# Performance work log

Measured on AMD Instinct MI355X. Metric: run time of the kernel, lower is better.

The kernel has to match this reference:

```python
import jax, jax.numpy as jnp
import numpy as np

B, T, D_IN, D, OUT, L, NDAYS = 32, 2048, 512, 256, 41, 3, 45
INNER = 2 * D  # expand=2

def silu(x):
    return x * jax.nn.sigmoid(x)

def layernorm(x, s, b, eps=1e-5):
    m = x.mean(-1, keepdims=True)
    v = ((x - m) ** 2).mean(-1, keepdims=True)
    return (x - m) / jnp.sqrt(v + eps) * s + b

def dwconv(x, k, b):
    # x: [B,T,C], k: [C,4] depthwise kernel, b: [C]
    # torch Conv1d(padding=2)[..., :T] == pad (left=2, right=1), valid window 4
    y = jax.lax.conv_general_dilated(
        x.transpose(0, 2, 1), k[:, None, :], window_strides=(1,),
        padding=[(2, 1)], feature_group_count=k.shape[0],
        dimension_numbers=('NCH', 'OIH', 'NCH'))
    return y.transpose(0, 2, 1) + b

def soft_window(x, Win, convK, convB, dtW, dtB, Wout):
    # x: [B,T,D]
    xz = x @ Win                      # [B,T,2*INNER]
    xi, z = jnp.split(xz, 2, axis=-1)
    xc = silu(dwconv(xi, convK, convB))
    dt = jax.nn.softplus(xc @ dtW + dtB)
    w = jnp.exp(-jnp.cumsum(dt, axis=1) * 0.1)
    return (xc * w * silu(z)) @ Wout  # [B,T,D]

def setup_inputs() -> dict:
    key = jax.random.key(0)
    ks = iter(jax.random.split(key, 40))
    n = lambda shp, s=0.02: jax.random.normal(next(ks), shp, dtype=jnp.float32) * s
    inp = {}
    inp['x'] = jax.random.normal(next(ks), (B, T, D_IN), dtype=jnp.float32)
    inp['day_ids'] = jax.random.randint(next(ks), (B,), 0, NDAYS)
    inp['adapter_W'] = jnp.tile(jnp.eye(D_IN)[None], (NDAYS, 1, 1)) + n((NDAYS, D_IN, D_IN))
    inp['adapter_b'] = n((NDAYS, D_IN))
    inp['cW1'] = n((D_IN, D)); inp['cb1'] = n((D,))
    inp['cln1_s'] = jnp.ones((D,)); inp['cln1_b'] = jnp.zeros((D,))
    inp['cW2'] = n((D, D)); inp['cb2'] = n((D,))
    inp['cln2_s'] = jnp.ones((D,)); inp['cln2_b'] = jnp.zeros((D,))
    # mamba params: leading dims [L, 2] for (fwd, bwd) directions
    inp['m_in'] = n((L, 2, D, 2 * INNER))
    inp['m_convK'] = n((L, 2, INNER, 4), 0.2); inp['m_convB'] = n((L, 2, INNER))
    inp['m_dtW'] = n((L, 2, INNER, INNER)); inp['m_dtB'] = n((L, 2, INNER))
    inp['m_out'] = n((L, 2, INNER, D))
    inp['proj_W'] = n((L, 2 * D, D)); inp['proj_b'] = n((L, D))
    inp['norm_s'] = jnp.ones((L, D)); inp['norm_b'] = jnp.zeros((L, D))
    inp['outW'] = n((D, OUT)); inp['outb'] = n((OUT,))
    return inp

def reference(x, day_ids, adapter_W, adapter_b, cW1, cb1, cln1_s, cln1_b,
              cW2, cb2, cln2_s, cln2_b, m_in, m_convK, m_convB, m_dtW, m_dtB,
              m_out, proj_W, proj_b, norm_s, norm_b, outW, outb):
    # Day adapter: batched gather-matmul (replaces per-sample python loop)
    h = jnp.einsum('btd,bde->bte', x, adapter_W[day_ids]) + adapter_b[day_ids][:, None, :]
    h = jax.nn.soft_sign(h)
    # input compress MLP (dropout = eval identity)
    h = silu(layernorm(h @ cW1 + cb1, cln1_s, cln1_b))
    h = silu(layernorm(h @ cW2 + cb2, cln2_s, cln2_b))
    # stacked bidirectional pseudo-SSM layers
    for l in range(L):
        fwd = soft_window(h, m_in[l, 0], m_convK[l, 0], m_convB[l, 0],
                          m_dtW[l, 0], m_dtB[l, 0], m_out[l, 0])
        hr = h[:, ::-1, :]
        bwd = soft_window(hr, m_in[l, 1], m_convK[l, 1], m_convB[l, 1],
                          m_dtW[l, 1], m_dtB[l, 1], m_out[l, 1])[:, ::-1, :]
        combined = jnp.concatenate([fwd, bwd], axis=-1) @ proj_W[l] + proj_b[l]
        h = layernorm(h + combined, norm_s[l], norm_b[l])
    return jax.nn.log_softmax(h @ outW + outb, axis=-1)
```

## Files before the change

kernel.cpp:

```cpp
#include <hip/hip_runtime.h>
#include <hip/hip_bf16.h>
#include <cstdint>
#include <math.h>

typedef __bf16 bf16_t;
typedef bf16_t bf16x8 __attribute__((ext_vector_type(8)));
typedef bf16_t bf16x4 __attribute__((ext_vector_type(4)));
typedef float f32x4 __attribute__((ext_vector_type(4)));

#define B_ 32
#define T_ 2048
#define D_ 256
#define INNER_ 512
#define L_ 3
#define CHUNK_ 64
#define NCHUNK_ (T_/CHUNK_)

typedef const __attribute__((address_space(1))) void* gas_t;
typedef __attribute__((address_space(3))) void* las_t;
__device__ __forceinline__ void gll16(const void* g, void* l) {
  __builtin_amdgcn_global_load_lds((gas_t)g, (las_t)l, 16, 0, 0);
}

struct GemmP {
  const bf16_t* A;
  const bf16_t* Bt;
  const float* bias;
  float* outF;
  bf16_t* outB;
  const int* day_ids;
  long bStrideBt;
  int bStrideBias;
  int K, N, ldout, colOff, act, revA, revC, nValid;
};

__global__ __launch_bounds__(256, 4)
void gemm_kernel(GemmP p) {
  __shared__ bf16_t As[2*128*32];
  __shared__ bf16_t Bs[2*128*32];
  const int tid = threadIdx.x;
  const int wave = tid >> 6, lane = tid & 63;

  const int nb = p.N >> 7;
  const int nbs = __builtin_ctz(nb);
  const int c8 = blockIdx.x & 7;
  const int k8 = blockIdx.x >> 3;
  const int mGrp = (gridDim.x >> 3) >> nbs;
  const int m0 = (c8 * mGrp + (k8 >> nbs)) << 7;
  const int n0 = (k8 & (nb - 1)) << 7;

  const bf16_t* Bt = p.Bt;
  const float* bias = p.bias;
  if (p.day_ids) {
    int day = p.day_ids[m0 >> 11];
    Bt += (long)day * p.bStrideBt;
    if (bias) bias += (long)day * p.bStrideBias;
  }
  const int K = p.K;
  const int srow = tid >> 2;
  const int sc = ((tid & 3) - (tid >> 4)) & 3;
  const int sk = sc << 3;

  int ar0 = m0 + srow, ar1 = m0 + srow + 64;
  if (p.revA) {
    int t0 = ar0 & (T_-1); ar0 = ar0 - t0 + (T_-1 - t0);
    int t1 = ar1 & (T_-1); ar1 = ar1 - t1 + (T_-1 - t1);
  }
  const bf16_t* aP0 = p.A + (long)ar0 * K + sk;
  const bf16_t* aP1 = p.A + (long)ar1 * K + sk;
  const bf16_t* bP0 = Bt + (long)(n0 + srow) * K + sk;
  const bf16_t* bP1 = bP0 + (long)64 * K;

  char* aL = (char*)As + wave * 1024;
  char* bL = (char*)Bs + wave * 1024;

  f32x4 acc[4][4] = {};
  const int mw = ((wave >> 1) << 6), nw = ((wave & 1) << 6);
  const int fr = lane & 15;
  const int foff = (((lane >> 4) + (fr >> 2)) & 3) << 4;

  gll16(aP0, aL);
  gll16(aP1, aL + 4096);
  gll16(bP0, bL);
  gll16(bP1, bL + 4096);
  __syncthreads();

  const int nIter = K >> 5;
  for (int it = 0; it < nIter; ++it) {
    const int cur = (it & 1) << 13;
    const int nxt = cur ^ 8192;
    if (it + 1 < nIter) {
      const int k1 = (it + 1) << 5;
      gll16(aP0 + k1, aL + nxt);
      gll16(aP1 + k1, aL + nxt + 4096);
      gll16(bP0 + k1, bL + nxt);
      gll16(bP1 + k1, bL + nxt + 4096);
    }
    bf16x8 af[4], bfr[4];
#pragma unroll
    for (int i = 0; i < 4; i++)
      af[i] = *(const bf16x8*)((char*)As + cur + (mw + i*16 + fr)*64 + foff);
#pragma unroll
    for (int j = 0; j < 4; j++)
      bfr[j] = *(const bf16x8*)((char*)Bs + cur + (nw + j*16 + fr)*64 + foff);
#pragma unroll
    for (int i = 0; i < 4; i++)
#pragma unroll
      for (int j = 0; j < 4; j++)
        acc[i][j] = __builtin_amdgcn_mfma_f32_16x16x32_bf16(af[i], bfr[j], acc[i][j], 0, 0, 0);
    __syncthreads();
  }

  const int cn = lane & 15, rq = (lane >> 4) << 2;
#pragma unroll
  for (int i = 0; i < 4; i++) {
#pragma unroll
    for (int r = 0; r < 4; r++) {
      int gr = m0 + mw + i*16 + rq + r;
      int orow = gr;
      if (p.revC) { int t = gr & (T_-1); orow = gr - t + (T_-1 - t); }
      long rowOff = (long)orow * p.ldout + p.colOff;
#pragma unroll
      for (int j = 0; j < 4; j++) {
        int col = n0 + nw + j*16 + cn;
        if (col >= p.nValid) continue;
        float v = acc[i][j][r];
        if (bias) v += bias[col];
        if (p.act == 1) {
          v = v / (1.f + fabsf(v));
        } else if (p.act == 2) {
          float e = __expf(-fabsf(v));
          v = fmaxf(v, 0.f) + __logf(1.f + e);
        }
        if (p.outF) p.outF[rowOff + col] = v;
        if (p.outB) p.outB[rowOff + col] = (bf16_t)v;
      }
    }
  }
}

__global__ __launch_bounds__(256)
void ln_kernel(const bf16_t* in, const bf16_t* resid, const float* s, const float* bb,
               bf16_t* outB, int doSilu) {
  int row = (blockIdx.x << 2) + (threadIdx.x >> 6);
  int lane = threadIdx.x & 63;
  long base = (long)row * D_ + (lane << 2);
  bf16x4 iv = *(const bf16x4*)(in + base);
  float v[4];
#pragma unroll
  for (int k = 0; k < 4; k++) v[k] = (float)iv[k];
  if (resid) {
    bf16x4 rv = *(const bf16x4*)(resid + base);
#pragma unroll
    for (int k = 0; k < 4; k++) v[k] += (float)rv[k];
  }
  float s1 = v[0] + v[1] + v[2] + v[3];
  float s2 = v[0]*v[0] + v[1]*v[1] + v[2]*v[2] + v[3]*v[3];
#pragma unroll
  for (int off = 1; off < 64; off <<= 1) {
    s1 += __shfl_xor(s1, off);
    s2 += __shfl_xor(s2, off);
  }
  float mean = s1 * (1.f / D_);
  float var = s2 * (1.f / D_) - mean * mean;
  float inv = rsqrtf(var + 1e-5f);
  f32x4 sv = *(const f32x4*)(s + (lane << 2));
  f32x4 bv = *(const f32x4*)(bb + (lane << 2));
  bf16x4 ov;
#pragma unroll
  for (int k = 0; k < 4; k++) {
    float val = (v[k] - mean) * inv * sv[k] + bv[k];
    if (doSilu) val = val / (1.f + __expf(-val));
    ov[k] = (bf16_t)val;
  }
  *(bf16x4*)(outB + base) = ov;
}

__global__ __launch_bounds__(256)
void conv_kernel(const bf16_t* xz, const float* K4, const float* cb, bf16_t* xc) {
  long idx = (long)blockIdx.x * 256 + threadIdx.x;
  int ch0 = ((int)(idx & 63)) << 3;
  long bt = idx >> 6;
  int t = (int)(bt & (T_-1));
  const bf16_t* base = xz + bt * (2*INNER_) + ch0;
  bf16x8 r0, r1, r2, r3;
  r2 = *(const bf16x8*)(base);
#pragma unroll
  for (int k = 0; k < 8; k++) { r0[k] = (bf16_t)0.f; r1[k] = (bf16_t)0.f; r3[k] = (bf16_t)0.f; }
  if (t >= 2) r0 = *(const bf16x8*)(base - 2*(2*INNER_));
  if (t >= 1) r1 = *(const bf16x8*)(base - (2*INNER_));
  if (t < T_-1) r3 = *(const bf16x8*)(base + (2*INNER_));
  bf16x8 o8;
#pragma unroll
  for (int k = 0; k < 8; k++) {
    f32x4 kk = *(const f32x4*)(K4 + ((ch0 + k) << 2));
    float a = cb[ch0 + k] + (float)r0[k]*kk[0] + (float)r1[k]*kk[1]
            + (float)r2[k]*kk[2] + (float)r3[k]*kk[3];
    o8[k] = (bf16_t)(a / (1.f + __expf(-a)));
  }
  *(bf16x8*)(xc + bt * INNER_ + ch0) = o8;
}

__global__ __launch_bounds__(256)
void chunksum_kernel(const bf16_t* dt, float* sums) {
  int bc = blockIdx.x * 4 + (threadIdx.x >> 6);
  int ch0 = (threadIdx.x & 63) << 3;
  const bf16_t* p = dt + (long)bc * CHUNK_ * INNER_ + ch0;
  float a[8] = {};
  for (int i = 0; i < CHUNK_; i++) {
    bf16x8 v = *(const bf16x8*)(p + (long)i * INNER_);
#pragma unroll
    for (int k = 0; k < 8; k++) a[k] += (float)v[k];
  }
  float* o = sums + (long)bc * INNER_ + ch0;
#pragma unroll
  for (int k = 0; k < 8; k++) o[k] = a[k];
}

__global__ __launch_bounds__(256)
void y_kernel(const bf16_t* dt, const bf16_t* xz, bf16_t* xc, const float* sums) {
  int bc = blockIdx.x * 4 + (threadIdx.x >> 6);
  int b = bc >> 5;
  int c = bc & 31;
  int ch0 = (threadIdx.x & 63) << 3;
  float acc[8] = {};
  const float* sp = sums + (long)b * NCHUNK_ * INNER_ + ch0;
  for (int cp = 0; cp < c; cp++) {
#pragma unroll
    for (int k = 0; k < 8; k++) acc[k] += sp[(long)cp * INNER_ + k];
  }
  long bt0 = (long)bc * CHUNK_;
  for (int i = 0; i < CHUNK_; i++) {
    long bt = bt0 + i;
    bf16x8 d8 = *(const bf16x8*)(dt + bt * INNER_ + ch0);
    bf16x8 z8 = *(const bf16x8*)(xz + bt * (2*INNER_) + INNER_ + ch0);
    bf16x8 x8 = *(const bf16x8*)(xc + bt * INNER_ + ch0);
    bf16x8 o8;
#pragma unroll
    for (int k = 0; k < 8; k++) {
      acc[k] += (float)d8[k];
      float w = __expf(-0.1f * acc[k]);
      float zz = (float)z8[k];
      float sz = zz / (1.f + __expf(-zz));
      o8[k] = (bf16_t)((float)x8[k] * w * sz);
    }
    *(bf16x8*)(xc + bt * INNER_ + ch0) = o8;
  }
}

__global__ __launch_bounds__(256)
void lsm_kernel(const float* logits, float* out) {
  int row = (blockIdx.x << 2) + (threadIdx.x >> 6);
  int lane = threadIdx.x & 63;
  float v = (lane < 41) ? logits[(long)row * 41 + lane] : -3.4e38f;
  float m = v;
#pragma unroll
  for (int off = 1; off < 64; off <<= 1) m = fmaxf(m, __shfl_xor(m, off));
  float e = (lane < 41) ? __expf(v - m) : 0.f;
  float ssum = e;
#pragma unroll
  for (int off = 1; off < 64; off <<= 1) ssum += __shfl_xor(ssum, off);
  float ls = __logf(ssum);
  if (lane < 41) out[(long)row * 41 + lane] = v - m - ls;
}

__global__ void tconv_kernel(const float* in, bf16_t* out, int R, int C) {
  __shared__ float tile[32][33];
  const float* ip = in + (long)blockIdx.z * R * C;
  bf16_t* op = out + (long)blockIdx.z * R * C;
  int c0 = blockIdx.x << 5, r0 = blockIdx.y << 5;
  int tx = threadIdx.x, ty = threadIdx.y;
  for (int i = ty; i < 32; i += 8) {
    int r = r0 + i, c = c0 + tx;
    tile[i][tx] = (r < R && c < C) ? ip[(long)r * C + c] : 0.f;
  }
  __syncthreads();
  for (int i = ty; i < 32; i += 8) {
    int c = c0 + i, r = r0 + tx;
    if (c < C && r < R) op[(long)c * R + r] = (bf16_t)tile[tx][i];
  }
}

__global__ void cvt_kernel(const float* in, bf16_t* out, long n) {
  long i = ((long)blockIdx.x * blockDim.x + threadIdx.x) << 3;
  if (i >= n) return;
  f32x4 a = *(const f32x4*)(in + i);
  f32x4 b = *(const f32x4*)(in + i + 4);
  bf16x8 o;
#pragma unroll
  for (int k = 0; k < 4; k++) { o[k] = (bf16_t)a[k]; o[k+4] = (bf16_t)b[k]; }
  *(bf16x8*)(out + i) = o;
}

__global__ void zfill_kernel(bf16_t* p, int n) {
  int i = blockIdx.x * 256 + threadIdx.x;
  if (i < n) p[i] = (bf16_t)0.f;
}

extern "C" void kernel_launch(void* const* d_in, const int* in_sizes, int n_in,
                              void* d_out, int out_size, void* d_ws, size_t ws_size,
                              hipStream_t stream) {
  (void)in_sizes; (void)n_in; (void)out_size;
  const float* x         = (const float*)d_in[0];
  const int*   day_ids   = (const int*)d_in[1];
  const float* adapter_W = (const float*)d_in[2];
  const float* adapter_b = (const float*)d_in[3];
  const float* cW1       = (const float*)d_in[4];
  const float* cb1       = (const float*)d_in[5];
  const float* cln1_s    = (const float*)d_in[6];
  const float* cln1_b    = (const float*)d_in[7];
  const float* cW2       = (const float*)d_in[8];
  const float* cb2       = (const float*)d_in[9];
  const float* cln2_s    = (const float*)d_in[10];
  const float* cln2_b    = (const float*)d_in[11];
  const float* m_in      = (const float*)d_in[12];
  const float* m_convK   = (const float*)d_in[13];
  const float* m_convB   = (const float*)d_in[14];
  const float* m_dtW     = (const float*)d_in[15];
  const float* m_dtB     = (const float*)d_in[16];
  const float* m_out     = (const float*)d_in[17];
  const float* proj_W    = (const float*)d_in[18];
  const float* proj_b    = (const float*)d_in[19];
  const float* norm_s    = (const float*)d_in[20];
  const float* norm_b    = (const float*)d_in[21];
  const float* outW      = (const float*)d_in[22];
  const float* outb      = (const float*)d_in[23];
  float* out = (float*)d_out;

  char* ws = (char*)d_ws;
  size_t off = 0;
  auto alloc = [&](size_t bytes) -> char* {
    char* p = ws + off;
    off += (bytes + 255) & ~(size_t)255;
    return p;
  };
  bf16_t* adapterT = (bf16_t*)alloc((size_t)45*512*512*2);
  bf16_t* cW1T     = (bf16_t*)alloc((size_t)256*512*2);
  bf16_t* cW2T     = (bf16_t*)alloc((size_t)256*256*2);
  bf16_t* m_inT    = (bf16_t*)alloc((size_t)6*1024*256*2);
  bf16_t* m_dtWT   = (bf16_t*)alloc((size_t)6*512*512*2);
  bf16_t* m_outT   = (bf16_t*)alloc((size_t)6*256*512*2);
  bf16_t* projT    = (bf16_t*)alloc((size_t)3*256*512*2);
  bf16_t* outWT    = (bf16_t*)alloc((size_t)128*256*2);

  int Bg = 0;
  {
    const int cands[6] = {32, 16, 8, 4, 2, 1};
    for (int ci = 0; ci < 6; ci++) {
      int c = cands[ci];
      size_t Mg = (size_t)c * T_;
      size_t need = Mg*2048 + 3*(Mg*1024) + Mg*512 + (size_t)c*NCHUNK_*INNER_*4
                    + 8*256;
      if (off + need <= ws_size) { Bg = c; break; }
    }
  }
  if (Bg == 0) return;
  const size_t Mg = (size_t)Bg * T_;
  char*  xzR  = alloc(Mg * 2048);
  char*  xcR  = alloc(Mg * 1024);
  char*  dtR  = alloc(Mg * 1024);
  char*  swR  = alloc(Mg * 1024);
  bf16_t* hG  = (bf16_t*)alloc(Mg * 512);
  float* sums = (float*)alloc((size_t)Bg * NCHUNK_ * INNER_ * 4);

  zfill_kernel<<<128, 256, 0, stream>>>(outWT, 128*256);
  dim3 tb(32, 8);
  tconv_kernel<<<dim3(16,16,45), tb, 0, stream>>>(adapter_W, adapterT, 512, 512);
  tconv_kernel<<<dim3(8,16,1),  tb, 0, stream>>>(cW1,  cW1T,  512, 256);
  tconv_kernel<<<dim3(8,8,1),   tb, 0, stream>>>(cW2,  cW2T,  256, 256);
  tconv_kernel<<<dim3(32,8,6),  tb, 0, stream>>>(m_in, m_inT, 256, 1024);
  tconv_kernel<<<dim3(16,16,6), tb, 0, stream>>>(m_dtW, m_dtWT, 512, 512);
  tconv_kernel<<<dim3(8,16,6),  tb, 0, stream>>>(m_out, m_outT, 512, 256);
  tconv_kernel<<<dim3(8,16,3),  tb, 0, stream>>>(proj_W, projT, 512, 256);
  tconv_kernel<<<dim3(2,8,1),   tb, 0, stream>>>(outW, outWT, 256, 41);

  auto gemm = [&](const bf16_t* A, const bf16_t* Bt, const float* bias,
                  float* outF, bf16_t* outB, int K, int N, int ldout, int colOff,
                  int act, int revA, int revC, const int* days, long bsBt, int bsBias,
                  int nValid) {
    GemmP p;
    p.A = A; p.Bt = Bt; p.bias = bias; p.outF = outF; p.outB = outB;
    p.day_ids = days; p.bStrideBt = bsBt; p.bStrideBias = bsBias;
    p.K = K; p.N = N; p.ldout = ldout; p.colOff = colOff;
    p.act = act; p.revA = revA; p.revC = revC; p.nValid = nValid;
    gemm_kernel<<<dim3((unsigned)((Mg/128) * (N/128))), 256, 0, stream>>>(p);
  };

  for (int b0 = 0; b0 < B_; b0 += Bg) {
    const float* xg = x + (size_t)b0 * T_ * 512;

    bf16_t* x_bf = (bf16_t*)xzR;
    cvt_kernel<<<(unsigned)(Mg/4), 256, 0, stream>>>(xg, x_bf, (long)Mg*512);

    bf16_t* h0 = (bf16_t*)xcR;
    gemm(x_bf, adapterT, adapter_b, nullptr, h0, 512, 512, 512, 0, 1, 0, 0,
         day_ids + b0, (long)512*512, 512, 512);

    bf16_t* tmpB = (bf16_t*)dtR;
    gemm(h0, cW1T, cb1, nullptr, tmpB, 512, 256, 256, 0, 0, 0, 0, nullptr, 0, 0, 256);
    bf16_t* h1 = (bf16_t*)swR;
    ln_kernel<<<(unsigned)(Mg/4), 256, 0, stream>>>(tmpB, nullptr, cln1_s, cln1_b, h1, 1);

    gemm(h1, cW2T, cb2, nullptr, tmpB, 256, 256, 256, 0, 0, 0, 0, nullptr, 0, 0, 256);
    ln_kernel<<<(unsigned)(Mg/4), 256, 0, stream>>>(tmpB, nullptr, cln2_s, cln2_b, hG, 1);

    bf16_t* xz    = (bf16_t*)xzR;
    bf16_t* xc    = (bf16_t*)xcR;
    bf16_t* dt    = (bf16_t*)dtR;
    bf16_t* swcat = (bf16_t*)swR;

    for (int l = 0; l < L_; l++) {
      for (int dir = 0; dir < 2; dir++) {
        int ld = l*2 + dir;
        gemm(hG, m_inT + (size_t)ld*1024*256, nullptr, nullptr, xz,
             256, 1024, 1024, 0, 0, dir, 0, nullptr, 0, 0, 1024);
        conv_kernel<<<(unsigned)(Mg/4), 256, 0, stream>>>(
            xz, m_convK + (size_t)ld*512*4, m_convB + (size_t)ld*512, xc);
        gemm(xc, m_dtWT + (size_t)ld*512*512, m_dtB + (size_t)ld*512, nullptr, dt,
             512, 512, 512, 0, 2, 0, 0, nullptr, 0, 0, 512);
        chunksum_kernel<<<(unsigned)(Bg*8), 256, 0, stream>>>(dt, sums);
        y_kernel<<<(unsigned)(Bg*8), 256, 0, stream>>>(dt, xz, xc, sums);
        gemm(xc, m_outT + (size_t)ld*256*512, nullptr, nullptr, swcat,
             512, 256, 512, dir*256, 0, 0, dir, nullptr, 0, 0, 256);
      }
      bf16_t* tmpB2 = (bf16_t*)dtR;
      gemm(swcat, projT + (size_t)l*256*512, proj_b + (size_t)l*256, nullptr, tmpB2,
           512, 256, 256, 0, 0, 0, 0, nullptr, 0, 0, 256);
      ln_kernel<<<(unsigned)(Mg/4), 256, 0, stream>>>(tmpB2, hG, norm_s + (size_t)l*256,
                                                      norm_b + (size_t)l*256, hG, 0);
    }

    float* logits = (float*)xzR;
    gemm(hG, outWT, outb, logits, nullptr, 256, 128, 41, 0, 0, 0, 0,
         nullptr, 0, 0, 41);
    lsm_kernel<<<(unsigned)(Mg/4), 256, 0, stream>>>(logits, out + (size_t)b0 * T_ * 41);
  }
}
```

Baseline: 2.731 ms.

## Fuse dt chunk sums into GEMM epilogue and vectorize epilogue stores

Swaps the MFMA operand order so each lane holds four consecutive output columns of one row. This allows 4-wide bf16 stores and vector bias loads in the GEMM epilogue. A new act mode computes softplus and also reduces per-64-row chunk sums with lane shuffles, writing them to the sums buffer, which removes the separate chunksum kernel and its re-read of dt. It assumes each wave's 64-row M tile aligns with one chunk, and the bf16 stores now skip the nValid check.

Result: faster. 2.543 ms (-6.9%).

```diff
diff --git a/kernel.cpp b/kernel.cpp
--- a/kernel.cpp
+++ b/kernel.cpp
@@ -28,6 +28,7 @@
   const float* bias;
   float* outF;
   bf16_t* outB;
+  float* sums;
   const int* day_ids;
   long bStrideBt;
   int bStrideBias;
@@ -104,37 +105,73 @@
     for (int j = 0; j < 4; j++)
       bfr[j] = *(const bf16x8*)((char*)Bs + cur + (nw + j*16 + fr)*64 + foff);
 #pragma unroll
-    for (int i = 0; i < 4; i++)
-#pragma unroll
-      for (int j = 0; j < 4; j++)
-        acc[i][j] = __builtin_amdgcn_mfma_f32_16x16x32_bf16(af[i], bfr[j], acc[i][j], 0, 0, 0);
+    for (int im = 0; im < 4; im++)
+#pragma unroll
+      for (int in = 0; in < 4; in++)
+        acc[im][in] = __builtin_amdgcn_mfma_f32_16x16x32_bf16(bfr[in], af[im], acc[im][in], 0, 0, 0);
     __syncthreads();
   }
 
   const int cn = lane & 15, rq = (lane >> 4) << 2;
-#pragma unroll
-  for (int i = 0; i < 4; i++) {
-#pragma unroll
-    for (int r = 0; r < 4; r++) {
-      int gr = m0 + mw + i*16 + rq + r;
-      int orow = gr;
-      if (p.revC) { int t = gr & (T_-1); orow = gr - t + (T_-1 - t); }
-      long rowOff = (long)orow * p.ldout + p.colOff;
-#pragma unroll
-      for (int j = 0; j < 4; j++) {
-        int col = n0 + nw + j*16 + cn;
-        if (col >= p.nValid) continue;
-        float v = acc[i][j][r];
-        if (bias) v += bias[col];
-        if (p.act == 1) {
-          v = v / (1.f + fabsf(v));
-        } else if (p.act == 2) {
-          float e = __expf(-fabsf(v));
-          v = fmaxf(v, 0.f) + __logf(1.f + e);
+  f32x4 csum[4];
+#pragma unroll
+  for (int in = 0; in < 4; in++) csum[in] = (f32x4){0.f,0.f,0.f,0.f};
+
+#pragma unroll
+  for (int im = 0; im < 4; im++) {
+    int gr = m0 + mw + im*16 + cn;
+    int orow = gr;
+    if (p.revC) { int t = gr & (T_-1); orow = gr - t + (T_-1 - t); }
+    long rowOff = (long)orow * p.ldout + p.colOff;
+#pragma unroll
+    for (int in = 0; in < 4; in++) {
+      int colb = n0 + nw + in*16 + rq;
+      f32x4 v = acc[im][in];
+      if (bias) {
+        f32x4 bv = *(const f32x4*)(bias + colb);
+        v = v + bv;
+      }
+      if (p.act == 1) {
+#pragma unroll
+        for (int r = 0; r < 4; r++) v[r] = v[r] / (1.f + fabsf(v[r]));
+      } else if (p.act >= 2) {
+#pragma unroll
+        for (int r = 0; r < 4; r++) {
+          float e = __expf(-fabsf(v[r]));
+          v[r] = fmaxf(v[r], 0.f) + __logf(1.f + e);
         }
-        if (p.outF) p.outF[rowOff + col] = v;
-        if (p.outB) p.outB[rowOff + col] = (bf16_t)v;
-      }
+      }
+      if (p.act == 3) csum[in] = csum[in] + v;
+      if (p.outB) {
+        bf16x4 o;
+#pragma unroll
+        for (int r = 0; r < 4; r++) o[r] = (bf16_t)v[r];
+        *(bf16x4*)(p.outB + rowOff + colb) = o;
+      }
+      if (p.outF) {
+#pragma unroll
+        for (int r = 0; r < 4; r++) {
+          int col = colb + r;
+          if (col < p.nValid) p.outF[rowOff + col] = v[r];
+        }
+      }
+    }
+  }
+
+  if (p.act == 3) {
+#pragma unroll
+    for (int in = 0; in < 4; in++) {
+#pragma unroll
+      for (int b = 1; b < 16; b <<= 1) {
+#pragma unroll
+        for (int r = 0; r < 4; r++) csum[in][r] += __shfl_xor(csum[in][r], b);
+      }
+    }
+    if (cn == 0) {
+      int chunk = (m0 + mw) >> 6;
+#pragma unroll
+      for (int in = 0; in < 4; in++)
+        *(f32x4*)(p.sums + (long)chunk * INNER_ + n0 + nw + in*16 + rq) = csum[in];
     }
   }
 }
@@ -199,22 +236,6 @@
     o8[k] = (bf16_t)(a / (1.f + __expf(-a)));
   }
   *(bf16x8*)(xc + bt * INNER_ + ch0) = o8;
-}
-
-__global__ __launch_bounds__(256)
-void chunksum_kernel(const bf16_t* dt, float* sums) {
-  int bc = blockIdx.x * 4 + (threadIdx.x >> 6);
-  int ch0 = (threadIdx.x & 63) << 3;
-  const bf16_t* p = dt + (long)bc * CHUNK_ * INNER_ + ch0;
-  float a[8] = {};
-  for (int i = 0; i < CHUNK_; i++) {
-    bf16x8 v = *(const bf16x8*)(p + (long)i * INNER_);
-#pragma unroll
-    for (int k = 0; k < 8; k++) a[k] += (float)v[k];
-  }
-  float* o = sums + (long)bc * INNER_ + ch0;
-#pragma unroll
-  for (int k = 0; k < 8; k++) o[k] = a[k];
 }
 
 __global__ __launch_bounds__(256)
@@ -377,9 +398,9 @@
   auto gemm = [&](const bf16_t* A, const bf16_t* Bt, const float* bias,
                   float* outF, bf16_t* outB, int K, int N, int ldout, int colOff,
                   int act, int revA, int revC, const int* days, long bsBt, int bsBias,
-                  int nValid) {
+                  int nValid, float* sumsP) {
     GemmP p;
-    p.A = A; p.Bt = Bt; p.bias = bias; p.outF = outF; p.outB = outB;
+    p.A = A; p.Bt = Bt; p.bias = bias; p.outF = outF; p.outB = outB; p.sums = sumsP;
     p.day_ids = days; p.bStrideBt = bsBt; p.bStrideBias = bsBias;
     p.K = K; p.N = N; p.ldout = ldout; p.colOff = colOff;
     p.act = act; p.revA = revA; p.revC = revC; p.nValid = nValid;
@@ -394,14 +415,14 @@
 
     bf16_t* h0 = (bf16_t*)xcR;
     gemm(x_bf, adapterT, adapter_b, nullptr, h0, 512, 512, 512, 0, 1, 0, 0,
-         day_ids + b0, (long)512*512, 512, 512);
+         day_ids + b0, (long)512*512, 512, 512, nullptr);
 
     bf16_t* tmpB = (bf16_t*)dtR;
-    gemm(h0, cW1T, cb1, nullptr, tmpB, 512, 256, 256, 0, 0, 0, 0, nullptr, 0, 0, 256);
+    gemm(h0, cW1T, cb1, nullptr, tmpB, 512, 256, 256, 0, 0, 0, 0, nullptr, 0, 0, 256, nullptr);
     bf16_t* h1 = (bf16_t*)swR;
     ln_kernel<<<(unsigned)(Mg/4), 256, 0, stream>>>(tmpB, nullptr, cln1_s, cln1_b, h1, 1);
 
-    gemm(h1, cW2T, cb2, nullptr, tmpB, 256, 256, 256, 0, 0, 0, 0, nullptr, 0, 0, 256);
+    gemm(h1, cW2T, cb2, nullptr, tmpB, 256, 256, 256, 0, 0, 0, 0, nullptr, 0, 0, 256, nullptr);
     ln_kernel<<<(unsigned)(Mg/4), 256, 0, stream>>>(tmpB, nullptr, cln2_s, cln2_b, hG, 1);
 
     bf16_t* xz    = (bf16_t*)xzR;
@@ -413,26 +434,25 @@
       for (int dir = 0; dir < 2; dir++) {
         int ld = l*2 + dir;
         gemm(hG, m_inT + (size_t)ld*1024*256, nullptr, nullptr, xz,
-             256, 1024, 1024, 0, 0, dir, 0, nullptr, 0, 0, 1024);
+             256, 1024, 1024, 0, 0, dir, 0, nullptr, 0, 0, 1024, nullptr);
         conv_kernel<<<(unsigned)(Mg/4), 256, 0, stream>>>(
             xz, m_convK + (size_t)ld*512*4, m_convB + (size_t)ld*512, xc);
         gemm(xc, m_dtWT + (size_t)ld*512*512, m_dtB + (size_t)ld*512, nullptr, dt,
-             512, 512, 512, 0, 2, 0, 0, nullptr, 0, 0, 512);
-        chunksum_kernel<<<(unsigned)(Bg*8), 256, 0, stream>>>(dt, sums);
+             512, 512, 512, 0, 3, 0, 0, nullptr, 0, 0, 512, sums);
         y_kernel<<<(unsigned)(Bg*8), 256, 0, stream>>>(dt, xz, xc, sums);
         gemm(xc, m_outT + (size_t)ld*256*512, nullptr, nullptr, swcat,
-             512, 256, 512, dir*256, 0, 0, dir, nullptr, 0, 0, 256);
+             512, 256, 512, dir*256, 0, 0, dir, nullptr, 0, 0, 256, nullptr);
       }
       bf16_t* tmpB2 = (bf16_t*)dtR;
       gemm(swcat, projT + (size_t)l*256*512, proj_b + (size_t)l*256, nullptr, tmpB2,
-           512, 256, 256, 0, 0, 0, 0, nullptr, 0, 0, 256);
+           512, 256, 256, 0, 0, 0, 0, nullptr, 0, 0, 256, nullptr);
       ln_kernel<<<(unsigned)(Mg/4), 256, 0, stream>>>(tmpB2, hG, norm_s + (size_t)l*256,
                                                       norm_b + (size_t)l*256, hG, 0);
     }
 
     float* logits = (float*)xzR;
     gemm(hG, outWT, outb, logits, nullptr, 256, 128, 41, 0, 0, 0, 0,
-         nullptr, 0, 0, 41);
+         nullptr, 0, 0, 41, nullptr);
     lsm_kernel<<<(unsigned)(Mg/4), 256, 0, stream>>>(logits, out + (size_t)b0 * T_ * 41);
   }
 }
```
